# Optimization experiments

Measured on AMD Instinct MI355X. Metric: run time of the kernel, lower is better.

The kernel has to match this reference:

```python
import jax, jax.numpy as jnp
import numpy as np

KV_SIZE = 512


def setup_inputs() -> dict:
    key = jax.random.key(0)
    k1, k2, k3 = jax.random.split(key, 3)
    B, T, C = 8, 4096, 1024
    x = jax.random.normal(k1, (B, T, C), dtype=jnp.float32)
    k_t_1 = jax.random.normal(k2, (B, KV_SIZE, C), dtype=jnp.float32)
    v_t_1 = jax.random.normal(k3, (B, KV_SIZE, C), dtype=jnp.float32)
    return {"x": x, "k_t_1": k_t_1, "v_t_1": v_t_1}


def reference(x, k_t_1, v_t_1):
    # x: [B, T, C]; latent state k_t_1, v_t_1: [B, S=512, C]
    B, T, C = x.shape
    scale = 1.0 / jnp.sqrt(jnp.asarray(C, dtype=x.dtype))

    # Read: queries (tokens) attend over the fixed-size latent KV state.
    scores = jnp.einsum("btc,bsc->bts", x, k_t_1) * scale      # [B, T, S]
    att = jnp.einsum("bts,bsc->btc", jax.nn.softmax(scores, axis=-1), v_t_1)

    # Update: each latent slot attends over the incoming tokens and
    # accumulates the summary into the state (fixed-size KV cache update).
    k_scores = jnp.einsum("bsc,btc->bst", k_t_1, x) * scale     # [B, S, T]
    k_t = k_t_1 + jnp.einsum("bst,btc->bsc", jax.nn.softmax(k_scores, axis=-1), x)
    v_scores = jnp.einsum("bsc,btc->bst", v_t_1, x) * scale     # [B, S, T]
    v_t = v_t_1 + jnp.einsum("bst,btc->bsc", jax.nn.softmax(v_scores, axis=-1), x)

    return att, k_t, v_t
```

## Files before the change

### kernel.cpp

```cpp
#include <hip/hip_runtime.h>
#include <hip/hip_bf16.h>

#define BB 8
#define TT 4096
#define CC 1024
#define SS 512

typedef __bf16 bf16x8 __attribute__((ext_vector_type(8)));
typedef float f32x4 __attribute__((ext_vector_type(4)));
typedef unsigned short u16x8 __attribute__((ext_vector_type(8)));

__device__ __forceinline__ float bf2f(unsigned short u) {
  union { unsigned int i; float f; } x; x.i = ((unsigned int)u) << 16; return x.f;
}
__device__ __forceinline__ unsigned short f2bf(float f) {
  __hip_bfloat16 h = __float2bfloat16(f);
  unsigned short u; __builtin_memcpy(&u, &h, 2); return u;
}

__global__ void cvt_transpose(const float* __restrict__ in,
                              unsigned short* __restrict__ out_rm,
                              unsigned short* __restrict__ out_t,
                              float* __restrict__ out_f32,
                              int R, int Cd) {
  __shared__ float tile[64][65];
  const long bo = (long)blockIdx.z * R * Cd;
  const int r0 = blockIdx.x * 64, c0 = blockIdx.y * 64;
  const int tx = threadIdx.x, ty = threadIdx.y;
#pragma unroll
  for (int i = 0; i < 16; ++i) {
    int r = ty + i * 4;
    float v = in[bo + (long)(r0 + r) * Cd + c0 + tx];
    tile[r][tx] = v;
    out_rm[bo + (long)(r0 + r) * Cd + c0 + tx] = f2bf(v);
    if (out_f32 != nullptr) out_f32[bo + (long)(r0 + r) * Cd + c0 + tx] = v;
  }
  if (out_t != nullptr) {
    __syncthreads();
#pragma unroll
    for (int i = 0; i < 16; ++i) {
      int c = ty + i * 4;
      out_t[bo + (long)(c0 + c) * R + r0 + tx] = f2bf(tile[tx][c]);
    }
  }
}

__global__ void transpose_bf16(const unsigned short* __restrict__ in,
                               unsigned short* __restrict__ out,
                               int Rin, int Cin, long sIn, long sOut) {
  __shared__ unsigned short tile[64][72];
  const long bi = (long)blockIdx.z * sIn;
  const long bo = (long)blockIdx.z * sOut;
  const int r0 = blockIdx.x * 64, c0 = blockIdx.y * 64;
  const int tid = threadIdx.x;
  const int lr = tid >> 3;
  const int lc = (tid & 7) * 8;
#pragma unroll
  for (int p = 0; p < 2; ++p) {
    int r = lr + p * 32;
    *(u16x8*)&tile[r][lc] = *(const u16x8*)&in[bi + (long)(r0 + r) * Cin + c0 + lc];
  }
  __syncthreads();
#pragma unroll
  for (int p = 0; p < 2; ++p) {
    int s = lr + p * 32;
    u16x8 val;
#pragma unroll
    for (int j = 0; j < 8; ++j) val[j] = tile[lc + j][s];
    *(u16x8*)&out[bo + (long)(c0 + s) * Rin + r0 + lc] = val;
  }
}

template <int ROWLEN>
__global__ __launch_bounds__(256) void row_softmax(unsigned short* __restrict__ sc) {
  constexpr int NV = ROWLEN / 512;
  const int lane = threadIdx.x & 63;
  const long row = (long)blockIdx.x * 4 + (threadIdx.x >> 6);
  unsigned short* base = sc + row * (long)ROWLEN;
  u16x8 d[NV];
  float m = -1e30f;
#pragma unroll
  for (int v = 0; v < NV; ++v) {
    d[v] = *(const u16x8*)&base[(v * 64 + lane) * 8];
#pragma unroll
    for (int j = 0; j < 8; ++j) m = fmaxf(m, bf2f(d[v][j]));
  }
#pragma unroll
  for (int off = 32; off >= 1; off >>= 1) m = fmaxf(m, __shfl_xor(m, off, 64));
  float l = 0.f;
#pragma unroll
  for (int v = 0; v < NV; ++v) {
#pragma unroll
    for (int j = 0; j < 8; ++j) {
      float e = __expf(bf2f(d[v][j]) - m);
      l += e;
      d[v][j] = f2bf(e);
    }
  }
#pragma unroll
  for (int off = 32; off >= 1; off >>= 1) l += __shfl_xor(l, off, 64);
  const float inv = 1.f / l;
#pragma unroll
  for (int v = 0; v < NV; ++v) {
    u16x8 o;
#pragma unroll
    for (int j = 0; j < 8; ++j) o[j] = f2bf(bf2f(d[v][j]) * inv);
    *(u16x8*)&base[(v * 64 + lane) * 8] = o;
  }
}

template <bool OUT_BF16, bool ATOMIC>
__global__ __launch_bounds__(256) void gemm_bt(
    const unsigned short* __restrict__ A,
    const unsigned short* __restrict__ A2, int lda, long sA,
    const unsigned short* __restrict__ Bt, int ldb, long sB,
    void* __restrict__ Cout, void* __restrict__ Cout2, int ldc, long sC,
    float alpha, int M, int N, int K, int halfM, int kshift) {
  __shared__ unsigned short As[128 * 64];
  __shared__ unsigned short Bs[128 * 64];
  const int zb = blockIdx.z >> kshift;
  const int kch = blockIdx.z & ((1 << kshift) - 1);
  const int Kc = K >> kshift;
  const int kstart = kch * Kc;
  const int kend = kstart + Kc;
  const int m0full = blockIdx.y * 128;
  const bool hi = m0full >= halfM;
  const unsigned short* Ab = ((hi && A2 != nullptr) ? A2 : A) + (long)zb * sA;
  const int mA = (hi && A2 != nullptr) ? m0full - halfM : m0full;
  void* Cbase = (hi && Cout2 != nullptr) ? Cout2 : Cout;
  const int mC = (hi && Cout2 != nullptr) ? m0full - halfM : m0full;
  const unsigned short* Bb = Bt + (long)zb * sB;
  const int n0 = blockIdx.x * 128;
  const int tid = threadIdx.x;
  const int lane = tid & 63;
  const int wm = (tid >> 6) & 1;
  const int wn = tid >> 7;
  const int srow = tid >> 3;
  const int scol = (tid & 7) * 8;
  f32x4 zero = {0.f, 0.f, 0.f, 0.f};
  f32x4 acc[4][4];
#pragma unroll
  for (int i = 0; i < 4; ++i)
#pragma unroll
    for (int j = 0; j < 4; ++j) acc[i][j] = zero;

  for (int k0 = kstart; k0 < kend; k0 += 64) {
#pragma unroll
    for (int p = 0; p < 4; ++p) {
      int r = srow + p * 32;
      const unsigned short* g = Ab + (long)(mA + r) * lda + k0 + scol;
      __builtin_amdgcn_global_load_lds(
          (const __attribute__((address_space(1))) void*)g,
          (__attribute__((address_space(3))) void*)&As[r * 64 + scol], 16, 0, 0);
    }
#pragma unroll
    for (int p = 0; p < 4; ++p) {
      int r = srow + p * 32;
      const unsigned short* g = Bb + (long)(n0 + r) * ldb + k0 + scol;
      __builtin_amdgcn_global_load_lds(
          (const __attribute__((address_space(1))) void*)g,
          (__attribute__((address_space(3))) void*)&Bs[r * 64 + scol], 16, 0, 0);
    }
    __syncthreads();
#pragma unroll
    for (int kk = 0; kk < 2; ++kk) {
      const int kof = kk * 32 + (lane >> 4) * 8;
      bf16x8 af[4], bfr[4];
#pragma unroll
      for (int i = 0; i < 4; ++i)
        af[i] = *(const bf16x8*)&As[(wm * 64 + i * 16 + (lane & 15)) * 64 + kof];
#pragma unroll
      for (int j = 0; j < 4; ++j)
        bfr[j] = *(const bf16x8*)&Bs[(wn * 64 + j * 16 + (lane & 15)) * 64 + kof];
#pragma unroll
      for (int i = 0; i < 4; ++i)
#pragma unroll
        for (int j = 0; j < 4; ++j)
          acc[i][j] = __builtin_amdgcn_mfma_f32_16x16x32_bf16(af[i], bfr[j], acc[i][j], 0, 0, 0);
    }
    __syncthreads();
  }
  const int rbase = (lane >> 4) * 4;
  const int cl = lane & 15;
#pragma unroll
  for (int i = 0; i < 4; ++i)
#pragma unroll
    for (int j = 0; j < 4; ++j)
#pragma unroll
      for (int r = 0; r < 4; ++r) {
        int row = mC + wm * 64 + i * 16 + rbase + r;
        int col = n0 + wn * 64 + j * 16 + cl;
        long idx = (long)zb * sC + (long)row * ldc + col;
        float v = acc[i][j][r] * alpha;
        if (ATOMIC) {
          unsafeAtomicAdd(&((float*)Cbase)[idx], v);
        } else if (OUT_BF16) {
          ((unsigned short*)Cbase)[idx] = f2bf(v);
        } else {
          ((float*)Cbase)[idx] = v;
        }
      }
}

extern "C" void kernel_launch(void* const* d_in, const int* in_sizes, int n_in,
                              void* d_out, int out_size, void* d_ws, size_t ws_size,
                              hipStream_t stream) {
  const float* x = (const float*)d_in[0];
  const float* kin = (const float*)d_in[1];
  const float* vin = (const float*)d_in[2];

  float* att = (float*)d_out;
  float* kt = att + (long)BB * TT * CC;
  float* vt = kt + (long)BB * SS * CC;

  unsigned short* xb = (unsigned short*)d_out;
  unsigned short* xT = xb + (long)BB * TT * CC;

  const float scale = 0.03125f;
  dim3 cblk(64, 4);
  const long MiB = 1024 * 1024;

  if (ws_size >= (size_t)(104 * MiB)) {
    char* w = (char*)d_ws;
    unsigned short* sc  = (unsigned short*)w;
    unsigned short* kb  = (unsigned short*)w;
    unsigned short* vb  = (unsigned short*)(w + 8 * MiB);
    unsigned short* vT  = (unsigned short*)(w + 32 * MiB);
    unsigned short* pkv = (unsigned short*)(w + 40 * MiB);

    cvt_transpose<<<dim3(TT / 64, CC / 64, BB), cblk, 0, stream>>>(x, xb, xT, nullptr, TT, CC);
    cvt_transpose<<<dim3(SS / 64, CC / 64, BB), cblk, 0, stream>>>(kin, kb, nullptr, kt, SS, CC);
    cvt_transpose<<<dim3(SS / 64, CC / 64, BB), cblk, 0, stream>>>(vin, vb, vT, vt, SS, CC);

    gemm_bt<true, false><<<dim3(TT / 128, 2 * SS / 128, BB), 256, 0, stream>>>(
        kb, vb, CC, (long)SS * CC, xb, CC, (long)TT * CC,
        pkv, nullptr, TT, (long)2 * SS * TT, scale, 2 * SS, TT, CC, SS, 0);

    transpose_bf16<<<dim3(SS / 64, TT / 64, BB), 256, 0, stream>>>(
        pkv, sc, SS, TT, (long)2 * SS * TT, (long)TT * SS);

    row_softmax<TT><<<BB * 2 * SS / 4, 256, 0, stream>>>(pkv);

    gemm_bt<false, true><<<dim3(CC / 128, 2 * SS / 128, BB * 2), 256, 0, stream>>>(
        pkv, nullptr, TT, (long)2 * SS * TT, xT, TT, (long)CC * TT,
        kt, vt, CC, (long)SS * CC, 1.f, 2 * SS, CC, TT, SS, 1);

    row_softmax<SS><<<BB * TT / 4, 256, 0, stream>>>(sc);

    gemm_bt<false, false><<<dim3(CC / 128, TT / 128, BB), 256, 0, stream>>>(
        sc, nullptr, SS, (long)TT * SS, vT, SS, (long)CC * SS,
        att, nullptr, CC, (long)TT * CC, 1.f, TT, CC, SS, 1 << 30, 0);
  } else {
    char* w = (char*)d_ws;
    unsigned short* kb = (unsigned short*)w;
    unsigned short* vb = (unsigned short*)(w + 8 * MiB);
    unsigned short* vT = (unsigned short*)(w + 16 * MiB);
    unsigned short* sc = (unsigned short*)(w + 24 * MiB);
    unsigned short* pk = (unsigned short*)(w + 56 * MiB);

    cvt_transpose<<<dim3(TT / 64, CC / 64, BB), cblk, 0, stream>>>(x, xb, xT, nullptr, TT, CC);
    cvt_transpose<<<dim3(SS / 64, CC / 64, BB), cblk, 0, stream>>>(kin, kb, nullptr, kt, SS, CC);
    cvt_transpose<<<dim3(SS / 64, CC / 64, BB), cblk, 0, stream>>>(vin, vb, vT, vt, SS, CC);

    gemm_bt<true, false><<<dim3(TT / 128, SS / 128, BB), 256, 0, stream>>>(
        kb, nullptr, CC, (long)SS * CC, xb, CC, (long)TT * CC,
        pk, nullptr, TT, (long)SS * TT, scale, SS, TT, CC, 1 << 30, 0);
    transpose_bf16<<<dim3(SS / 64, TT / 64, BB), 256, 0, stream>>>(
        pk, sc, SS, TT, (long)SS * TT, (long)TT * SS);
    row_softmax<TT><<<BB * SS / 4, 256, 0, stream>>>(pk);
    gemm_bt<false, true><<<dim3(CC / 128, SS / 128, BB * 4), 256, 0, stream>>>(
        pk, nullptr, TT, (long)SS * TT, xT, TT, (long)CC * TT,
        kt, nullptr, CC, (long)SS * CC, 1.f, SS, CC, TT, 1 << 30, 2);

    gemm_bt<true, false><<<dim3(TT / 128, SS / 128, BB), 256, 0, stream>>>(
        vb, nullptr, CC, (long)SS * CC, xb, CC, (long)TT * CC,
        pk, nullptr, TT, (long)SS * TT, scale, SS, TT, CC, 1 << 30, 0);
    row_softmax<TT><<<BB * SS / 4, 256, 0, stream>>>(pk);
    gemm_bt<false, true><<<dim3(CC / 128, SS / 128, BB * 4), 256, 0, stream>>>(
        pk, nullptr, TT, (long)SS * TT, xT, TT, (long)CC * TT,
        vt, nullptr, CC, (long)SS * CC, 1.f, SS, CC, TT, 1 << 30, 2);

    row_softmax<SS><<<BB * TT / 4, 256, 0, stream>>>(sc);
    gemm_bt<false, false><<<dim3(CC / 128, TT / 128, BB), 256, 0, stream>>>(
        sc, nullptr, SS, (long)TT * SS, vT, SS, (long)CC * SS,
        att, nullptr, CC, (long)TT * CC, 1.f, TT, CC, SS, 1 << 30, 0);
  }
}
```

Baseline: 700.2 us.

## Replace GEMM with 256x256-tile, 4-slot LDS-pipelined kernel and XCD block remap

Replaces the 128x128 single-buffered GEMM with a 512-thread kernel that computes 256x256 output tiles. It streams 32-wide K slices into a 4-slot ring in dynamic LDS (128 KB) via global_load_lds, prefetching two slices ahead. LDS addresses are XOR-swizzled to avoid bank conflicts, and MFMA phases run at raised wave priority. Block indices are remapped across 8 chunks so that neighbouring tiles land on the same XCD and share L2. The intent is higher data reuse per tile and overlap of global loads with MFMA work. The cost is fewer blocks per launch, only one block per CU because of the LDS footprint, and hand-written waitcnt/barrier sequencing that is fragile.

```diff
diff --git a/kernel.cpp b/kernel.cpp
--- a/kernel.cpp
+++ b/kernel.cpp
@@ -110,85 +110,136 @@
 }
 
 template <bool OUT_BF16, bool ATOMIC>
-__global__ __launch_bounds__(256) void gemm_bt(
+__global__ __launch_bounds__(512, 2) void gemm256(
     const unsigned short* __restrict__ A,
     const unsigned short* __restrict__ A2, int lda, long sA,
     const unsigned short* __restrict__ Bt, int ldb, long sB,
     void* __restrict__ Cout, void* __restrict__ Cout2, int ldc, long sC,
     float alpha, int M, int N, int K, int halfM, int kshift) {
-  __shared__ unsigned short As[128 * 64];
-  __shared__ unsigned short Bs[128 * 64];
-  const int zb = blockIdx.z >> kshift;
-  const int kch = blockIdx.z & ((1 << kshift) - 1);
+  extern __shared__ unsigned char lds[];
+
+  const int gx = gridDim.x, gy = gridDim.y;
+  int nx = blockIdx.x, ny = blockIdx.y, nz = blockIdx.z;
+  {
+    const int total = gx * gy * gridDim.z;
+    if ((total & 7) == 0) {
+      int flat = blockIdx.x + gx * (blockIdx.y + gy * blockIdx.z);
+      const int chunk = total >> 3;
+      flat = (flat & 7) * chunk + (flat >> 3);
+      ny = flat % gy;
+      nx = (flat / gy) % gx;
+      nz = flat / (gy * gx);
+    }
+  }
+
+  const int zb = nz >> kshift;
+  const int kch = nz & ((1 << kshift) - 1);
   const int Kc = K >> kshift;
   const int kstart = kch * Kc;
-  const int kend = kstart + Kc;
-  const int m0full = blockIdx.y * 128;
+  const int nt = Kc >> 5;
+  const int m0full = ny * 256;
   const bool hi = m0full >= halfM;
   const unsigned short* Ab = ((hi && A2 != nullptr) ? A2 : A) + (long)zb * sA;
   const int mA = (hi && A2 != nullptr) ? m0full - halfM : m0full;
   void* Cbase = (hi && Cout2 != nullptr) ? Cout2 : Cout;
   const int mC = (hi && Cout2 != nullptr) ? m0full - halfM : m0full;
   const unsigned short* Bb = Bt + (long)zb * sB;
-  const int n0 = blockIdx.x * 128;
+  const int n0 = nx * 256;
+
   const int tid = threadIdx.x;
   const int lane = tid & 63;
-  const int wm = (tid >> 6) & 1;
-  const int wn = tid >> 7;
-  const int srow = tid >> 3;
-  const int scol = (tid & 7) * 8;
-  f32x4 zero = {0.f, 0.f, 0.f, 0.f};
-  f32x4 acc[4][4];
-#pragma unroll
-  for (int i = 0; i < 4; ++i)
-#pragma unroll
-    for (int j = 0; j < 4; ++j) acc[i][j] = zero;
-
-  for (int k0 = kstart; k0 < kend; k0 += 64) {
-#pragma unroll
-    for (int p = 0; p < 4; ++p) {
-      int r = srow + p * 32;
-      const unsigned short* g = Ab + (long)(mA + r) * lda + k0 + scol;
-      __builtin_amdgcn_global_load_lds(
-          (const __attribute__((address_space(1))) void*)g,
-          (__attribute__((address_space(3))) void*)&As[r * 64 + scol], 16, 0, 0);
-    }
-#pragma unroll
-    for (int p = 0; p < 4; ++p) {
-      int r = srow + p * 32;
-      const unsigned short* g = Bb + (long)(n0 + r) * ldb + k0 + scol;
-      __builtin_amdgcn_global_load_lds(
-          (const __attribute__((address_space(1))) void*)g,
-          (__attribute__((address_space(3))) void*)&Bs[r * 64 + scol], 16, 0, 0);
-    }
-    __syncthreads();
-#pragma unroll
-    for (int kk = 0; kk < 2; ++kk) {
-      const int kof = kk * 32 + (lane >> 4) * 8;
-      bf16x8 af[4], bfr[4];
-#pragma unroll
-      for (int i = 0; i < 4; ++i)
-        af[i] = *(const bf16x8*)&As[(wm * 64 + i * 16 + (lane & 15)) * 64 + kof];
+  const int wid = tid >> 6;
+  const int wm = wid >> 2;
+  const int wn = wid & 3;
+  const int l15 = lane & 15;
+  const int skb = (((lane >> 4) ^ ((l15 >> 1) & 3)) << 4);
+  const int aoff = (wm * 128 + l15) * 64 + skb;
+  const int boff = (wn * 64 + l15) * 64 + skb;
+
+  const int srow = tid >> 2;
+  const int skb2 = ((tid & 3) << 4) ^ (((srow >> 1) & 3) << 4);
+
+#define STAGE_OP(gb, ld, r0, k0, ldsoff)                                      \
+  {                                                                           \
+    _Pragma("unroll")                                                         \
+    for (int i_ = 0; i_ < 2; ++i_) {                                          \
+      const unsigned short* g_ = (gb) + (long)((r0) + i_ * 128 + srow) * (ld) \
+                                 + (k0) + (skb2 >> 1);                        \
+      __builtin_amdgcn_global_load_lds(                                       \
+          (const __attribute__((address_space(1))) void*)g_,                  \
+          (__attribute__((address_space(3))) void*)(lds + (ldsoff) +          \
+                                                    i_ * 8192 + tid * 16),    \
+          16, 0, 0);                                                          \
+    }                                                                         \
+  }
+
+  f32x4 acc[8][4];
+#pragma unroll
+  for (int i = 0; i < 8; ++i)
+#pragma unroll
+    for (int j = 0; j < 4; ++j) acc[i][j] = (f32x4){0.f, 0.f, 0.f, 0.f};
+
+  STAGE_OP(Ab, lda, mA, kstart, 0);
+  STAGE_OP(Bb, ldb, n0, kstart, 65536);
+  STAGE_OP(Ab, lda, mA, kstart + 32, 16384);
+  STAGE_OP(Bb, ldb, n0, kstart + 32, 65536 + 16384);
+  asm volatile("s_waitcnt vmcnt(4)" ::: "memory");
+  __builtin_amdgcn_s_barrier();
+
+  for (int t = 0; t < nt; ++t) {
+    const int slot = t & 3;
+    const unsigned char* Al = lds + slot * 16384;
+    const unsigned char* Bl = lds + 65536 + slot * 16384;
+    const int ts = t + 2;
+    const int ks = kstart + ((ts < nt) ? ts * 32 : 0);
+    const int ss = ts & 3;
+
+    bf16x8 bfr[4], af[4];
+#pragma unroll
+    for (int j = 0; j < 4; ++j) bfr[j] = *(const bf16x8*)(Bl + boff + j * 1024);
+#pragma unroll
+    for (int i = 0; i < 4; ++i) af[i] = *(const bf16x8*)(Al + aoff + i * 1024);
+    STAGE_OP(Ab, lda, mA, ks, ss * 16384);
+    __builtin_amdgcn_s_barrier();
+    asm volatile("s_waitcnt lgkmcnt(0)" ::: "memory");
+    __builtin_amdgcn_sched_barrier(0);
+    __builtin_amdgcn_s_setprio(1);
+#pragma unroll
+    for (int i = 0; i < 4; ++i)
 #pragma unroll
       for (int j = 0; j < 4; ++j)
-        bfr[j] = *(const bf16x8*)&Bs[(wn * 64 + j * 16 + (lane & 15)) * 64 + kof];
-#pragma unroll
-      for (int i = 0; i < 4; ++i)
-#pragma unroll
-        for (int j = 0; j < 4; ++j)
-          acc[i][j] = __builtin_amdgcn_mfma_f32_16x16x32_bf16(af[i], bfr[j], acc[i][j], 0, 0, 0);
-    }
-    __syncthreads();
-  }
+        acc[i][j] = __builtin_amdgcn_mfma_f32_16x16x32_bf16(af[i], bfr[j], acc[i][j], 0, 0, 0);
+    __builtin_amdgcn_s_setprio(0);
+    __builtin_amdgcn_s_barrier();
+
+    bf16x8 af2[4];
+#pragma unroll
+    for (int i = 0; i < 4; ++i) af2[i] = *(const bf16x8*)(Al + aoff + (i + 4) * 1024);
+    STAGE_OP(Bb, ldb, n0, ks, 65536 + ss * 16384);
+    __builtin_amdgcn_s_barrier();
+    asm volatile("s_waitcnt lgkmcnt(0)" ::: "memory");
+    __builtin_amdgcn_sched_barrier(0);
+    __builtin_amdgcn_s_setprio(1);
+#pragma unroll
+    for (int i = 0; i < 4; ++i)
+#pragma unroll
+      for (int j = 0; j < 4; ++j)
+        acc[i + 4][j] = __builtin_amdgcn_mfma_f32_16x16x32_bf16(af2[i], bfr[j], acc[i + 4][j], 0, 0, 0);
+    __builtin_amdgcn_s_setprio(0);
+    asm volatile("s_waitcnt vmcnt(4)" ::: "memory");
+    __builtin_amdgcn_s_barrier();
+  }
+#undef STAGE_OP
+
   const int rbase = (lane >> 4) * 4;
   const int cl = lane & 15;
 #pragma unroll
-  for (int i = 0; i < 4; ++i)
+  for (int i = 0; i < 8; ++i)
 #pragma unroll
     for (int j = 0; j < 4; ++j)
 #pragma unroll
       for (int r = 0; r < 4; ++r) {
-        int row = mC + wm * 64 + i * 16 + rbase + r;
+        int row = mC + wm * 128 + i * 16 + rbase + r;
         int col = n0 + wn * 64 + j * 16 + cl;
         long idx = (long)zb * sC + (long)row * ldc + col;
         float v = acc[i][j][r] * alpha;
@@ -209,6 +260,20 @@
   const float* kin = (const float*)d_in[1];
   const float* vin = (const float*)d_in[2];
 
+  static bool lds_opted = false;
+  if (!lds_opted) {
+    (void)hipFuncSetAttribute(
+        reinterpret_cast<const void*>(&gemm256<true, false>),
+        hipFuncAttributeMaxDynamicSharedMemorySize, 131072);
+    (void)hipFuncSetAttribute(
+        reinterpret_cast<const void*>(&gemm256<false, true>),
+        hipFuncAttributeMaxDynamicSharedMemorySize, 131072);
+    (void)hipFuncSetAttribute(
+        reinterpret_cast<const void*>(&gemm256<false, false>),
+        hipFuncAttributeMaxDynamicSharedMemorySize, 131072);
+    lds_opted = true;
+  }
+
   float* att = (float*)d_out;
   float* kt = att + (long)BB * TT * CC;
   float* vt = kt + (long)BB * SS * CC;
@@ -219,6 +284,7 @@
   const float scale = 0.03125f;
   dim3 cblk(64, 4);
   const long MiB = 1024 * 1024;
+  const int GLDS = 131072;
 
   if (ws_size >= (size_t)(104 * MiB)) {
     char* w = (char*)d_ws;
@@ -232,7 +298,7 @@
     cvt_transpose<<<dim3(SS / 64, CC / 64, BB), cblk, 0, stream>>>(kin, kb, nullptr, kt, SS, CC);
     cvt_transpose<<<dim3(SS / 64, CC / 64, BB), cblk, 0, stream>>>(vin, vb, vT, vt, SS, CC);
 
-    gemm_bt<true, false><<<dim3(TT / 128, 2 * SS / 128, BB), 256, 0, stream>>>(
+    gemm256<true, false><<<dim3(TT / 256, 2 * SS / 256, BB), 512, GLDS, stream>>>(
         kb, vb, CC, (long)SS * CC, xb, CC, (long)TT * CC,
         pkv, nullptr, TT, (long)2 * SS * TT, scale, 2 * SS, TT, CC, SS, 0);
 
@@ -241,13 +307,13 @@
 
     row_softmax<TT><<<BB * 2 * SS / 4, 256, 0, stream>>>(pkv);
 
-    gemm_bt<false, true><<<dim3(CC / 128, 2 * SS / 128, BB * 2), 256, 0, stream>>>(
+    gemm256<false, true><<<dim3(CC / 256, 2 * SS / 256, BB * 2), 512, GLDS, stream>>>(
         pkv, nullptr, TT, (long)2 * SS * TT, xT, TT, (long)CC * TT,
         kt, vt, CC, (long)SS * CC, 1.f, 2 * SS, CC, TT, SS, 1);
 
     row_softmax<SS><<<BB * TT / 4, 256, 0, stream>>>(sc);
 
-    gemm_bt<false, false><<<dim3(CC / 128, TT / 128, BB), 256, 0, stream>>>(
+    gemm256<false, false><<<dim3(CC / 256, TT / 256, BB), 512, GLDS, stream>>>(
         sc, nullptr, SS, (long)TT * SS, vT, SS, (long)CC * SS,
         att, nullptr, CC, (long)TT * CC, 1.f, TT, CC, SS, 1 << 30, 0);
   } else {
@@ -262,26 +328,26 @@
     cvt_transpose<<<dim3(SS / 64, CC / 64, BB), cblk, 0, stream>>>(kin, kb, nullptr, kt, SS, CC);
     cvt_transpose<<<dim3(SS / 64, CC / 64, BB), cblk, 0, stream>>>(vin, vb, vT, vt, SS, CC);
 
-    gemm_bt<true, false><<<dim3(TT / 128, SS / 128, BB), 256, 0, stream>>>(
+    gemm256<true, false><<<dim3(TT / 256, SS / 256, BB), 512, GLDS, stream>>>(
         kb, nullptr, CC, (long)SS * CC, xb, CC, (long)TT * CC,
         pk, nullptr, TT, (long)SS * TT, scale, SS, TT, CC, 1 << 30, 0);
     transpose_bf16<<<dim3(SS / 64, TT / 64, BB), 256, 0, stream>>>(
         pk, sc, SS, TT, (long)SS * TT, (long)TT * SS);
     row_softmax<TT><<<BB * SS / 4, 256, 0, stream>>>(pk);
-    gemm_bt<false, true><<<dim3(CC / 128, SS / 128, BB * 4), 256, 0, stream>>>(
+    gemm256<false, true><<<dim3(CC / 256, SS / 256, BB * 4), 512, GLDS, stream>>>(
         pk, nullptr, TT, (long)SS * TT, xT, TT, (long)CC * TT,
         kt, nullptr, CC, (long)SS * CC, 1.f, SS, CC, TT, 1 << 30, 2);
 
-    gemm_bt<true, false><<<dim3(TT / 128, SS / 128, BB), 256, 0, stream>>>(
+    gemm256<true, false><<<dim3(TT / 256, SS / 256, BB), 512, GLDS, stream>>>(
         vb, nullptr, CC, (long)SS * CC, xb, CC, (long)TT * CC,
         pk, nullptr, TT, (long)SS * TT, scale, SS, TT, CC, 1 << 30, 0);
     row_softmax<TT><<<BB * SS / 4, 256, 0, stream>>>(pk);
-    gemm_bt<false, true><<<dim3(CC / 128, SS / 128, BB * 4), 256, 0, stream>>>(
+    gemm256<false, true><<<dim3(CC / 256, SS / 256, BB * 4), 512, GLDS, stream>>>(
         pk, nullptr, TT, (long)SS * TT, xT, TT, (long)CC * TT,
         vt, nullptr, CC, (long)SS * CC, 1.f, SS, CC, TT, 1 << 30, 2);
 
     row_softmax<SS><<<BB * TT / 4, 256, 0, stream>>>(sc);
-    gemm_bt<false, false><<<dim3(CC / 128, TT / 128, BB), 256, 0, stream>>>(
+    gemm256<false, false><<<dim3(CC / 256, TT / 256, BB), 512, GLDS, stream>>>(
         sc, nullptr, SS, (long)TT * SS, vT, SS, (long)CC * SS,
         att, nullptr, CC, (long)TT * CC, 1.f, TT, CC, SS, 1 << 30, 0);
   }
```

After: 602.6 us. 1.16x faster.
